# Optimization experiments

Measured on AMD Instinct MI355X. Metric: run time of the kernel, lower is better.

## Reference

```python
import jax, jax.numpy as jnp
import numpy as np

C = 1.0          # ball curvature (Manifold default)
EPS = 1e-7
MIN_NORM = 1e-15

def _artanh(x):
    return jnp.arctanh(jnp.clip(x, -1.0 + EPS, 1.0 - EPS))

def _expmap0(u):
    # exp map at origin of the Poincare ball
    n = jnp.clip(jnp.linalg.norm(u, axis=-1, keepdims=True), MIN_NORM, None)
    sc = np.sqrt(C).astype(np.float32)
    return jnp.tanh(sc * n) * u / (sc * n)

def _mobius_add(x, y):
    x2 = jnp.sum(x * x, axis=-1, keepdims=True)
    y2 = jnp.sum(y * y, axis=-1, keepdims=True)
    xy = jnp.sum(x * y, axis=-1, keepdims=True)
    num = (1.0 + 2.0 * C * xy + C * y2) * x + (1.0 - C * x2) * y
    den = 1.0 + 2.0 * C * xy + C * C * x2 * y2
    return num / jnp.clip(den, MIN_NORM, None)

def setup_inputs() -> dict:
    key = jax.random.key(0)
    k1, k2, k3, k4 = jax.random.split(key, 4)
    N, D, U = 8192, 256, 128
    features = jax.random.normal(k1, (N, D), jnp.float32) * 0.1
    adj = jax.random.randint(k2, (N, N), 0, 2, jnp.int32)
    kernel = jax.random.normal(k3, (D, U), jnp.float32) * (1.0 / np.sqrt(D)).astype(np.float32)
    bias = jax.random.normal(k4, (U,), jnp.float32) * 0.01
    return {"features": features, "adj": adj, "kernel": kernel, "bias": bias}

def reference(features, adj, kernel, bias):
    sc = np.sqrt(C).astype(np.float32)
    # dense matmul then lift to the ball
    x = _expmap0(features @ kernel)                     # [N, U]
    # pairwise hyperbolic distance via closed form of ||mobius_add(-x_i, x_j)||
    x2 = jnp.sum(x * x, axis=-1)                        # [N]
    xy = x @ x.T                                        # [N, N]
    A = 1.0 - 2.0 * C * xy + C * x2[None, :]            # [N, N]
    B = (1.0 - C * x2)[:, None]                         # [N, 1]
    num_sq = A * A * x2[:, None] - 2.0 * A * B * xy + B * B * x2[None, :]
    den = 1.0 - 2.0 * C * xy + C * C * x2[:, None] * x2[None, :]
    mnorm = jnp.sqrt(jnp.clip(num_sq, 0.0, None)) / jnp.clip(den, MIN_NORM, None)
    dist = (2.0 / sc) * _artanh(sc * mnorm)             # sqdist ** 0.5 == distance, [N, N]
    # adjacency-masked softmax (zeros -> -inf, as in tf.where(a != 0, a, float.min))
    a = dist * adj.astype(dist.dtype)
    a = jnp.where(a != 0, a, jnp.finfo(a.dtype).min)
    att = jax.nn.softmax(a, axis=-1)                    # [N, N]
    # mobius_matvec with exchange=True: hyperbolic analogue of att @ x (row-wise norm rescale)
    mx = att @ x                                        # [N, U]
    x_n = jnp.clip(jnp.sqrt(x2)[:, None], MIN_NORM, None)
    mx_n = jnp.clip(jnp.linalg.norm(mx, axis=-1, keepdims=True), MIN_NORM, None)
    out = jnp.tanh(mx_n / x_n * _artanh(sc * x_n)) * mx / (sc * mx_n)
    # hyperbolic bias
    b = _expmap0(bias[None, :])                         # [1, U]
    return _mobius_add(out, b)
```

## Files before the change

kernel.cpp:

```cpp
#include <hip/hip_runtime.h>
#include <hip/hip_bf16.h>
#include <math.h>

#define Nn 8192
#define Dd 256
#define Uu 128
#define MI 16
#define NJC 8
#define JCL (Nn / NJC)
#define NIT (JCL / 16)

typedef __attribute__((ext_vector_type(4))) float f32x4;
typedef __attribute__((ext_vector_type(8))) short s16x8;
typedef __attribute__((ext_vector_type(4))) short s16x4;

#define MFMA_K32(a, b, c) __builtin_amdgcn_mfma_f32_16x16x32_bf16((a), (b), (c), 0, 0, 0)

#define GL_LDS(src, dst)                                                              \
  __builtin_amdgcn_global_load_lds(                                                   \
      (const __attribute__((address_space(1))) unsigned int*)(src),                   \
      (__attribute__((address_space(3))) unsigned int*)(dst), 16, 0, 0)

__device__ __forceinline__ f32x4 mfma_k16(s16x4 a, s16x4 b, f32x4 c){
#if __has_builtin(__builtin_amdgcn_mfma_f32_16x16x16bf16_1k)
  return __builtin_amdgcn_mfma_f32_16x16x16bf16_1k(a, b, c, 0, 0, 0);
#else
  asm("v_mfma_f32_16x16x16_bf16 %0, %1, %2, %0" : "+v"(c) : "v"(a), "v"(b));
  return c;
#endif
}

__device__ __forceinline__ short f2bf(float f){
  unsigned int u = __float_as_uint(f);
  u += 0x7fffu + ((u >> 16) & 1u);
  return (short)(u >> 16);
}

__device__ __forceinline__ float waveSum(float v){
  #pragma unroll
  for (int off = 32; off >= 1; off >>= 1) v += __shfl_xor(v, off);
  return v;
}

__global__ __launch_bounds__(256) void k_prep(const float* __restrict__ feat,
                                              const float* __restrict__ kern,
                                              const float* __restrict__ bias,
                                              short* __restrict__ xh,
                                              short* __restrict__ v4,
                                              float* __restrict__ x2,
                                              float* __restrict__ bb){
  const int t = threadIdx.x;
  const int u = t & 127;
  const int g = t >> 7;
  const int n0 = blockIdx.x * 16;
  __shared__ float fS[16][Dd];
  __shared__ float red[4][8];
  __shared__ float redb[4];
  {
    const f32x4* fg = (const f32x4*)(feat + (size_t)n0 * Dd);
    f32x4* fd = (f32x4*)fS;
    #pragma unroll
    for (int c = 0; c < 4; ++c) fd[c * 256 + t] = fg[c * 256 + t];
  }
  __syncthreads();
  float zz[8];
  #pragma unroll
  for (int r = 0; r < 8; ++r) zz[r] = 0.f;
  for (int dq = 0; dq < 64; ++dq){
    const int d = dq * 4;
    const float k0 = kern[(size_t)(d + 0) * Uu + u];
    const float k1 = kern[(size_t)(d + 1) * Uu + u];
    const float k2 = kern[(size_t)(d + 2) * Uu + u];
    const float k3 = kern[(size_t)(d + 3) * Uu + u];
    #pragma unroll
    for (int r = 0; r < 8; ++r){
      const f32x4 f4 = *(const f32x4*)&fS[g * 8 + r][d];
      zz[r] = fmaf(f4.x, k0, fmaf(f4.y, k1, fmaf(f4.z, k2, fmaf(f4.w, k3, zz[r]))));
    }
  }
  #pragma unroll
  for (int r = 0; r < 8; ++r){
    float v = waveSum(zz[r] * zz[r]);
    if ((t & 63) == 0) red[t >> 6][r] = v;
  }
  __syncthreads();
  float scl[8];
  #pragma unroll
  for (int r = 0; r < 8; ++r){
    const float ns  = (g == 0) ? (red[0][r] + red[1][r]) : (red[2][r] + red[3][r]);
    const float nrm = fmaxf(sqrtf(ns), 1e-15f);
    const float th  = tanhf(nrm);
    scl[r] = th / nrm;
    xh[(size_t)(n0 + g * 8 + r) * Uu + u] = f2bf(zz[r] * scl[r]);
  }
  {
    short* vt = v4 + (size_t)blockIdx.x * 2048 + (size_t)(u >> 4) * 256 + (u & 15) * 4;
    #pragma unroll
    for (int qq = 0; qq < 2; ++qq){
      s16x4 w;
      #pragma unroll
      for (int e = 0; e < 4; ++e) w[e] = f2bf(zz[qq * 4 + e] * scl[qq * 4 + e]);
      *(s16x4*)(vt + (g * 2 + qq) * 64) = w;
    }
  }
  if (t < 16){
    const float ns  = (t < 8) ? (red[0][t] + red[1][t]) : (red[2][t - 8] + red[3][t - 8]);
    const float nrm = fmaxf(sqrtf(ns), 1e-15f);
    const float th  = tanhf(nrm);
    x2[n0 + t] = th * th;
  }
  if (blockIdx.x == 0){
    const float bv = (t < 128) ? bias[t] : 0.f;
    float v = waveSum(bv * bv);
    if ((t & 63) == 0) redb[t >> 6] = v;
    __syncthreads();
    const float n2  = redb[0] + redb[1] + redb[2] + redb[3];
    const float nrm = fmaxf(sqrtf(n2), 1e-15f);
    const float th  = tanhf(nrm);
    if (t < 128) bb[t] = bv * th / nrm;
    if (t == 0) bb[Uu] = th * th;
  }
}

__global__ __launch_bounds__(256, 4) void k_attn(const int* __restrict__ adj,
                                                 const short* __restrict__ xh,
                                                 const short* __restrict__ v4,
                                                 const float* __restrict__ x2g,
                                                 float* __restrict__ Opart,
                                                 float* __restrict__ lpart){
  const int t    = threadIdx.x;
  const int lane = t & 63;
  const int wid  = t >> 6;
  const int l15  = lane & 15;
  const int q4   = lane >> 4;
  const int ig   = blockIdx.x >> 3;
  const int jc   = blockIdx.x & 7;
  const int i0   = ig * 64 + wid * 16;
  const int irow = i0 + l15;
  const int jbase = jc * JCL;

  __shared__ __align__(16) short kb[2][2048];
  __shared__ __align__(16) short vb[2][2048];
  __shared__ __align__(16) float x2S[JCL];

  const char* ksrc = (const char*)xh + (size_t)jbase * 256
                     + (size_t)(lane & 15) * 256 + wid * 64 + (lane >> 4) * 16;
  const char* vsrc = (const char*)v4 + (size_t)jbase * 256 + wid * 1024 + lane * 16;

  GL_LDS(ksrc, (char*)&kb[0][0] + wid * 1024);
  GL_LDS(vsrc, (char*)&vb[0][0] + wid * 1024);
  GL_LDS((const char*)(x2g + jbase) + wid * 1024 + lane * 16, (char*)x2S + wid * 1024);

  s16x8 qf[4];
  {
    const short* qp = xh + (size_t)irow * Uu + q4 * 8;
    #pragma unroll
    for (int kk = 0; kk < 4; ++kk) qf[kk] = *(const s16x8*)(qp + kk * 32);
  }
  const float x2i  = x2g[irow];
  const float Bv   = 1.f - x2i;
  const float Bv2j = Bv * Bv;
  const float nBv2 = -2.f * Bv;

  f32x4 oc[8];
  #pragma unroll
  for (int uc = 0; uc < 8; ++uc) oc[uc] = (f32x4){0.f, 0.f, 0.f, 0.f};
  float lacc = 0.f;

  const int itDiag = ((i0 >> 10) == jc) ? ((i0 & 1023) >> 4) : -1;

  const int* ap = adj + (size_t)irow * Nn + jbase + q4 * 4;

  int4 aqA = *(const int4*)(ap);
  int4 aqB = *(const int4*)(ap + 16);
  int4 aqC = *(const int4*)(ap + 32);

  asm volatile("s_waitcnt vmcnt(0)" ::: "memory");
  __builtin_amdgcn_s_barrier();
  __builtin_amdgcn_sched_barrier(0);

  #pragma unroll 1
  for (int it = 0; it < NIT; ++it){
    const int cur = it & 1;
    if (it + 1 < NIT){
      GL_LDS(ksrc + (size_t)(it + 1) * 4096, (char*)&kb[cur ^ 1][0] + wid * 1024);
      GL_LDS(vsrc + (size_t)(it + 1) * 4096, (char*)&vb[cur ^ 1][0] + wid * 1024);
    }
    __builtin_amdgcn_sched_barrier(0);
    const int4 aqN = *(const int4*)(ap + (((it + 3 < NIT) ? (it + 3) : (NIT - 1)) << 4));

    s16x8 kf[4];
    #pragma unroll
    for (int kk = 0; kk < 4; ++kk)
      kf[kk] = *(const s16x8*)((const char*)&kb[cur][0] + kk * 1024 + lane * 16);
    s16x4 vf[8];
    #pragma unroll
    for (int uc = 0; uc < 8; ++uc)
      vf[uc] = *(const s16x4*)((const char*)&vb[cur][0] + uc * 512 + lane * 8);
    const f32x4 x2j = *(const f32x4*)&x2S[it * 16 + q4 * 4];

    f32x4 s = {0.f, 0.f, 0.f, 0.f};
    s = MFMA_K32(kf[0], qf[0], s);
    s = MFMA_K32(kf[1], qf[1], s);
    s = MFMA_K32(kf[2], qf[2], s);
    s = MFMA_K32(kf[3], qf[3], s);

    const int aarr[4] = {aqA.x, aqA.y, aqA.z, aqA.w};
    const bool dg = (it == itDiag);
    const int j0 = jbase + it * 16;
    s16x4 pb;
    #pragma unroll
    for (int r = 0; r < 4; ++r){
      const float xy  = s[r];
      const float x2v = x2j[r];
      const float Aa  = fmaf(-2.f, xy, 1.f + x2v);
      const float num = fmaf(Aa * Aa, x2i, fmaf(nBv2 * Aa, xy, Bv2j * x2v));
      const float den = fmaf(x2i, x2v, fmaf(-2.f, xy, 1.f));
      const float sq  = __builtin_amdgcn_sqrtf(fmaxf(num, 0.f));
      const float pd  = fmaxf(den - sq, 1e-30f);
      float p = fminf((den + sq) * __builtin_amdgcn_rcpf(pd), 2.0e7f);
      bool keep = (aarr[r] != 0) && (sq != 0.f);
      if (dg) keep = keep && ((j0 + 4 * q4 + r) != irow);
      p = keep ? p : 0.f;
      lacc += p;
      pb[r] = f2bf(p);
    }

    #pragma unroll
    for (int uc = 0; uc < 8; ++uc) oc[uc] = mfma_k16(vf[uc], pb, oc[uc]);

    aqA = aqB; aqB = aqC; aqC = aqN;
    asm volatile("s_waitcnt vmcnt(1)" ::: "memory");
    __builtin_amdgcn_s_barrier();
    __builtin_amdgcn_sched_barrier(0);
  }

  lacc += __shfl_xor(lacc, 16);
  lacc += __shfl_xor(lacc, 32);
  if (lane < 16) lpart[(size_t)jc * Nn + i0 + lane] = lacc;
  float* op = Opart + ((size_t)jc * Nn + irow) * Uu + q4 * 4;
  #pragma unroll
  for (int uc = 0; uc < 8; ++uc) *(f32x4*)(op + uc * 16) = oc[uc];
}

__global__ __launch_bounds__(256) void k_out(const float* __restrict__ Opart,
                                             const float* __restrict__ lpart,
                                             const float* __restrict__ x2g,
                                             const float* __restrict__ bb,
                                             float* __restrict__ out){
  const int t  = threadIdx.x;
  const int i0 = blockIdx.x * MI;
  const int er = t >> 4;
  const int ec = t & 15;
  float l = 0.f;
  #pragma unroll
  for (int c = 0; c < NJC; ++c) l += lpart[(size_t)c * Nn + i0 + er];
  const float linv = 1.f / fmaxf(l, 1e-30f);
  float mx[8]; float s2 = 0.f;
  #pragma unroll
  for (int k = 0; k < 8; ++k){
    float v = 0.f;
    #pragma unroll
    for (int c = 0; c < NJC; ++c)
      v += Opart[((size_t)c * Nn + i0 + er) * Uu + ec + 16 * k];
    v *= linv;
    mx[k] = v; s2 = fmaf(v, v, s2);
  }
  s2 += __shfl_xor(s2, 1); s2 += __shfl_xor(s2, 2);
  s2 += __shfl_xor(s2, 4); s2 += __shfl_xor(s2, 8);
  const float mx_n = fmaxf(sqrtf(s2), 1e-15f);
  const float x2e  = x2g[i0 + er];
  const float x_n  = fmaxf(sqrtf(x2e), 1e-15f);
  const float xcl  = fminf(x_n, 1.f - 1e-7f);
  const float art  = 0.5f * __logf((1.f + xcl) / (1.f - xcl));
  const float th   = tanhf(mx_n / x_n * art);
  const float rmn  = th / mx_n;
  float o[8], bu[8]; float ob = 0.f;
  #pragma unroll
  for (int k = 0; k < 8; ++k){
    bu[k] = bb[ec + 16 * k];
    o[k]  = mx[k] * rmn;
    ob = fmaf(o[k], bu[k], ob);
  }
  ob += __shfl_xor(ob, 1); ob += __shfl_xor(ob, 2);
  ob += __shfl_xor(ob, 4); ob += __shfl_xor(ob, 8);
  const float o2   = th * th;
  const float b2   = bb[Uu];
  const float cnum = 1.f + 2.f * ob + b2;
  const float cden = fmaf(o2, b2, 1.f + 2.f * ob);
  const float rden = 1.f / fmaxf(cden, 1e-15f);
  const float co   = 1.f - o2;
  #pragma unroll
  for (int k = 0; k < 8; ++k)
    out[(size_t)(i0 + er) * Uu + ec + 16 * k] = (cnum * o[k] + co * bu[k]) * rden;
}

extern "C" void kernel_launch(void* const* d_in, const int* in_sizes, int n_in,
                              void* d_out, int out_size, void* d_ws, size_t ws_size,
                              hipStream_t stream){
  (void)in_sizes; (void)n_in; (void)out_size; (void)ws_size;
  const float* feat = (const float*)d_in[0];
  const int*   adj  = (const int*)d_in[1];
  const float* kern = (const float*)d_in[2];
  const float* bias = (const float*)d_in[3];

  float* Opart = (float*)d_ws;
  float* lpart = Opart + (size_t)NJC * Nn * Uu;
  float* x2    = lpart + (size_t)NJC * Nn;
  float* bbw   = x2 + Nn;
  short* xh    = (short*)(bbw + 132);
  short* v4    = xh + (size_t)Nn * Uu;

  k_prep<<<Nn / 16, 256, 0, stream>>>(feat, kern, bias, xh, v4, x2, bbw);
  k_attn<<<(Nn / 64) * NJC, 256, 0, stream>>>(adj, xh, v4, x2, Opart, lpart);
  k_out <<<Nn / MI, 256, 0, stream>>>(Opart, lpart, x2, bbw, (float*)d_out);
}
```

Before: 472.6 us.

## Software-pipeline score MFMA one tile ahead of softmax and PV accumulation

Restructures the main attention loop so the QK^T MFMAs for tile it are issued while the distance/softmax math and PV MFMAs run on tile it-1, with a prologue and epilogue. V fragments, x2 values and the adjacency word are carried across iterations in registers. The adjacency prefetch depth drops from three tiles to one, and the wait now drains all outstanding loads (vmcnt(0)) each iteration. This raises register pressure and may expose global adjacency latency.

Result: no change. 467.4 us (-1.1%).

```diff
diff --git a/kernel.cpp b/kernel.cpp
--- a/kernel.cpp
+++ b/kernel.cpp
@@ -171,68 +171,128 @@
 
   const int* ap = adj + (size_t)irow * Nn + jbase + q4 * 4;
 
-  int4 aqA = *(const int4*)(ap);
-  int4 aqB = *(const int4*)(ap + 16);
-  int4 aqC = *(const int4*)(ap + 32);
+  int4 aqC = *(const int4*)(ap);
 
   asm volatile("s_waitcnt vmcnt(0)" ::: "memory");
   __builtin_amdgcn_s_barrier();
   __builtin_amdgcn_sched_barrier(0);
 
-  #pragma unroll 1
-  for (int it = 0; it < NIT; ++it){
-    const int cur = it & 1;
-    if (it + 1 < NIT){
-      GL_LDS(ksrc + (size_t)(it + 1) * 4096, (char*)&kb[cur ^ 1][0] + wid * 1024);
-      GL_LDS(vsrc + (size_t)(it + 1) * 4096, (char*)&vb[cur ^ 1][0] + wid * 1024);
-    }
-    __builtin_amdgcn_sched_barrier(0);
-    const int4 aqN = *(const int4*)(ap + (((it + 3 < NIT) ? (it + 3) : (NIT - 1)) << 4));
-
+  f32x4 sP;
+  s16x4 vfP[8];
+  f32x4 x2jP;
+  int4  aqL = *(const int4*)(ap + 16);
+  {
+    GL_LDS(ksrc + 4096, (char*)&kb[1][0] + wid * 1024);
+    GL_LDS(vsrc + 4096, (char*)&vb[1][0] + wid * 1024);
     s16x8 kf[4];
     #pragma unroll
     for (int kk = 0; kk < 4; ++kk)
-      kf[kk] = *(const s16x8*)((const char*)&kb[cur][0] + kk * 1024 + lane * 16);
-    s16x4 vf[8];
-    #pragma unroll
-    for (int uc = 0; uc < 8; ++uc)
-      vf[uc] = *(const s16x4*)((const char*)&vb[cur][0] + uc * 512 + lane * 8);
-    const f32x4 x2j = *(const f32x4*)&x2S[it * 16 + q4 * 4];
-
+      kf[kk] = *(const s16x8*)((const char*)&kb[0][0] + kk * 1024 + lane * 16);
     f32x4 s = {0.f, 0.f, 0.f, 0.f};
     s = MFMA_K32(kf[0], qf[0], s);
     s = MFMA_K32(kf[1], qf[1], s);
     s = MFMA_K32(kf[2], qf[2], s);
     s = MFMA_K32(kf[3], qf[3], s);
-
-    const int aarr[4] = {aqA.x, aqA.y, aqA.z, aqA.w};
-    const bool dg = (it == itDiag);
-    const int j0 = jbase + it * 16;
-    s16x4 pb;
+    sP = s;
+    #pragma unroll
+    for (int uc = 0; uc < 8; ++uc)
+      vfP[uc] = *(const s16x4*)((const char*)&vb[0][0] + uc * 512 + lane * 8);
+    x2jP = *(const f32x4*)&x2S[q4 * 4];
+    asm volatile("s_waitcnt vmcnt(0)" ::: "memory");
+    __builtin_amdgcn_s_barrier();
+    __builtin_amdgcn_sched_barrier(0);
+  }
+
+  #pragma unroll 1
+  for (int it = 1; it < NIT; ++it){
+    const int cur = it & 1;
+    if (it + 1 < NIT){
+      GL_LDS(ksrc + (size_t)(it + 1) * 4096, (char*)&kb[cur ^ 1][0] + wid * 1024);
+      GL_LDS(vsrc + (size_t)(it + 1) * 4096, (char*)&vb[cur ^ 1][0] + wid * 1024);
+    }
+    __builtin_amdgcn_sched_barrier(0);
+
+    s16x8 kf[4];
+    #pragma unroll
+    for (int kk = 0; kk < 4; ++kk)
+      kf[kk] = *(const s16x8*)((const char*)&kb[cur][0] + kk * 1024 + lane * 16);
+    f32x4 sN = {0.f, 0.f, 0.f, 0.f};
+    sN = MFMA_K32(kf[0], qf[0], sN);
+    sN = MFMA_K32(kf[1], qf[1], sN);
+    sN = MFMA_K32(kf[2], qf[2], sN);
+    sN = MFMA_K32(kf[3], qf[3], sN);
+
+    {
+      const int aarr[4] = {aqC.x, aqC.y, aqC.z, aqC.w};
+      float pv[4];
+      #pragma unroll
+      for (int r = 0; r < 4; ++r){
+        const float xy  = sP[r];
+        const float x2v = x2jP[r];
+        const float Aa  = fmaf(-2.f, xy, 1.f + x2v);
+        const float num = fmaf(Aa * Aa, x2i, fmaf(nBv2 * Aa, xy, Bv2j * x2v));
+        const float den = fmaf(x2i, x2v, fmaf(-2.f, xy, 1.f));
+        const float sq  = __builtin_amdgcn_sqrtf(fmaxf(num, 0.f));
+        const float pd  = fmaxf(den - sq, 1e-30f);
+        const float p   = fminf((den + sq) * __builtin_amdgcn_rcpf(pd), 2.0e7f);
+        const bool keep = (aarr[r] != 0) && (sq != 0.f);
+        pv[r] = keep ? p : 0.f;
+      }
+      if (it - 1 == itDiag){
+        const int j0 = jbase + (it - 1) * 16;
+        #pragma unroll
+        for (int r = 0; r < 4; ++r)
+          if ((j0 + 4 * q4 + r) == irow) pv[r] = 0.f;
+      }
+      lacc += (pv[0] + pv[1]) + (pv[2] + pv[3]);
+      s16x4 pb;
+      #pragma unroll
+      for (int r = 0; r < 4; ++r) pb[r] = f2bf(pv[r]);
+      #pragma unroll
+      for (int uc = 0; uc < 8; ++uc) oc[uc] = mfma_k16(vfP[uc], pb, oc[uc]);
+    }
+
+    #pragma unroll
+    for (int uc = 0; uc < 8; ++uc)
+      vfP[uc] = *(const s16x4*)((const char*)&vb[cur][0] + uc * 512 + lane * 8);
+    x2jP = *(const f32x4*)&x2S[it * 16 + q4 * 4];
+    sP = sN;
+    aqC = aqL;
+    aqL = *(const int4*)(ap + (((it + 1 < NIT) ? (it + 1) : (NIT - 1)) << 4));
+
+    asm volatile("s_waitcnt vmcnt(0)" ::: "memory");
+    __builtin_amdgcn_s_barrier();
+    __builtin_amdgcn_sched_barrier(0);
+  }
+
+  {
+    const int aarr[4] = {aqC.x, aqC.y, aqC.z, aqC.w};
+    float pv[4];
     #pragma unroll
     for (int r = 0; r < 4; ++r){
-      const float xy  = s[r];
-      const float x2v = x2j[r];
+      const float xy  = sP[r];
+      const float x2v = x2jP[r];
       const float Aa  = fmaf(-2.f, xy, 1.f + x2v);
       const float num = fmaf(Aa * Aa, x2i, fmaf(nBv2 * Aa, xy, Bv2j * x2v));
       const float den = fmaf(x2i, x2v, fmaf(-2.f, xy, 1.f));
       const float sq  = __builtin_amdgcn_sqrtf(fmaxf(num, 0.f));
       const float pd  = fmaxf(den - sq, 1e-30f);
-      float p = fminf((den + sq) * __builtin_amdgcn_rcpf(pd), 2.0e7f);
-      bool keep = (aarr[r] != 0) && (sq != 0.f);
-      if (dg) keep = keep && ((j0 + 4 * q4 + r) != irow);
-      p = keep ? p : 0.f;
-      lacc += p;
-      pb[r] = f2bf(p);
-    }
-
-    #pragma unroll
-    for (int uc = 0; uc < 8; ++uc) oc[uc] = mfma_k16(vf[uc], pb, oc[uc]);
-
-    aqA = aqB; aqB = aqC; aqC = aqN;
-    asm volatile("s_waitcnt vmcnt(1)" ::: "memory");
-    __builtin_amdgcn_s_barrier();
-    __builtin_amdgcn_sched_barrier(0);
+      const float p   = fminf((den + sq) * __builtin_amdgcn_rcpf(pd), 2.0e7f);
+      const bool keep = (aarr[r] != 0) && (sq != 0.f);
+      pv[r] = keep ? p : 0.f;
+    }
+    if (NIT - 1 == itDiag){
+      const int j0 = jbase + (NIT - 1) * 16;
+      #pragma unroll
+      for (int r = 0; r < 4; ++r)
+        if ((j0 + 4 * q4 + r) == irow) pv[r] = 0.f;
+    }
+    lacc += (pv[0] + pv[1]) + (pv[2] + pv[3]);
+    s16x4 pb;
+    #pragma unroll
+    for (int r = 0; r < 4; ++r) pb[r] = f2bf(pv[r]);
+    #pragma unroll
+    for (int uc = 0; uc < 8; ++uc) oc[uc] = mfma_k16(vfP[uc], pb, oc[uc]);
   }
 
   lacc += __shfl_xor(lacc, 16);
```
